# Kernel tuning notes

Measured on AMD Instinct MI355X. Metric: run time of the kernel, lower is better.

## Reference

```python
import jax, jax.numpy as jnp
import numpy as np

N, E = 10000, 160000          # nodes, support edges
CIN, COUT = 32, 32            # channels
R, B = 6, 1                   # radial rings, band limit
M = 2 * B + 1                 # angular frequencies (-B..B)
EPS = 1e-8
PI = float(np.pi)


def _cplx(a):
    # (..., 2) real -> complex64
    return jax.lax.complex(a[..., 0], a[..., 1])


def _reim(z):
    # complex -> (..., 2) real
    return jnp.stack([jnp.real(z), jnp.imag(z)], axis=-1)


def _field_conv(xc, edges, stenc, w, off):
    """FieldConv (ftype=1): real radial/angular weights with per-channel phase offsets.
    xc: (N,Cin) complex, stenc: (E,R,M) complex stencil (transport+quadrature pre-multiplied),
    w: (R,M,Cin,Cout) real, off: (Cin,Cout) phase offsets."""
    Wc = w * jax.lax.complex(jnp.cos(off), jnp.sin(off))[None, None]   # (R,M,Cin,Cout) complex
    src, tgt = edges[:, 0], edges[:, 1]
    # edge gather + complex stencil multiply: (E,R,M,Cin)
    contrib = stenc[:, :, :, None] * xc[src][:, None, None, :]
    # scatter-add to target nodes: (N,R,M,Cin)
    agg = jax.ops.segment_sum(contrib, tgt, num_segments=N)
    # dense per-node filter contraction
    return jnp.einsum('nrmc,rmcd->nd', agg, Wc)


def _tangent_nonlin(xc, b):
    # magnitude ReLU with learned bias, direction preserved (complex tangent features)
    mag = jnp.abs(xc)
    return (jax.nn.relu(mag + b) / jnp.maximum(mag, EPS)) * xc


def _forward(x, supp_edges, supp_sten, w1, off1, b1, w2, off2, b2, res_w):
    xc = _cplx(x)                # (N,CIN) complex64
    stenc = _cplx(supp_sten)     # (E,R,M) complex64
    h = _tangent_nonlin(_field_conv(xc, supp_edges, stenc, w1, off1), b1)
    h = _field_conv(h, supp_edges, stenc, w2, off2)
    y = _tangent_nonlin(xc @ _cplx(res_w) + h, b2)   # residual TangentLin + nonlin
    return _reim(y)              # (N,COUT,2) float32


def setup_inputs() -> dict:
    key = jax.random.key(0)
    ks = jax.random.split(key, 10)
    s1 = 1.0 / np.sqrt(R * M * CIN)
    s2 = 1.0 / np.sqrt(R * M * COUT)
    return {
        'x': jax.random.normal(ks[0], (N, CIN, 2), jnp.float32),
        'supp_edges': jax.random.randint(ks[1], (E, 2), 0, N),
        'supp_sten': 0.1 * jax.random.normal(ks[2], (E, R, M, 2), jnp.float32),
        'w1': s1 * jax.random.normal(ks[3], (R, M, CIN, COUT), jnp.float32),
        'off1': jax.random.uniform(ks[4], (CIN, COUT), jnp.float32, -PI, PI),
        'b1': 0.1 * jax.random.normal(ks[5], (COUT,), jnp.float32),
        'w2': s2 * jax.random.normal(ks[6], (R, M, COUT, COUT), jnp.float32),
        'off2': jax.random.uniform(ks[7], (COUT, COUT), jnp.float32, -PI, PI),
        'b2': 0.1 * jax.random.normal(ks[8], (COUT,), jnp.float32),
        'res_w': (1.0 / np.sqrt(CIN)) * jax.random.normal(ks[9], (CIN, COUT, 2), jnp.float32),
    }


def reference(x, supp_edges, supp_sten, w1, off1, b1, w2, off2, b2, res_w):
    return _forward(x, supp_edges, supp_sten, w1, off1, b1, w2, off2, b2, res_w)
```

## Files before the change

### kernel.cpp

```cpp
#include <hip/hip_runtime.h>
#include <hip/hip_bf16.h>

#define NN   10000
#define EE   160000
#define CINC 32
#define COUTC 32
#define RRR  6
#define MMM  3
#define RM   (RRR*MMM)
#define KK   (RM*CINC)
#define KE   608
#define NPB  4
#define CAP  64
#define AROW 624
#define WSZ  19456
#define EPSV 1e-8f

typedef __attribute__((ext_vector_type(8))) short bf16x8;
typedef __attribute__((ext_vector_type(4))) float f32x4;
typedef __attribute__((ext_vector_type(16))) float f32x16;

__device__ inline short f2bf(float f) {
    __hip_bfloat16 b = __float2bfloat16(f);
    union { __hip_bfloat16 b; short s; } u; u.b = b;
    return u.s;
}
__device__ inline float bf2f(unsigned short h) {
    return __uint_as_float(((unsigned)h) << 16);
}
__device__ inline uint2 packsplit(float re, float im) {
    unsigned short rh = (unsigned short)f2bf(re);
    unsigned short rl = (unsigned short)f2bf(re - bf2f(rh));
    unsigned short ih = (unsigned short)f2bf(im);
    unsigned short il = (unsigned short)f2bf(im - bf2f(ih));
    return make_uint2((unsigned)rh | ((unsigned)rl << 16),
                      (unsigned)ih | ((unsigned)il << 16));
}

__global__ void __launch_bounds__(256)
k_build(const int* __restrict__ edges, int* __restrict__ cursor,
        const float* __restrict__ w1, const float* __restrict__ off1,
        const float* __restrict__ w2, const float* __restrict__ off2,
        short* __restrict__ Wcb1, short* __restrict__ Wcb2,
        int2* __restrict__ sei,
        const float2* __restrict__ xc, uint2* __restrict__ xbf,
        const float2* __restrict__ resw)
{
    int i = blockIdx.x*blockDim.x + threadIdx.x;
    if (i < KK*COUTC) {
        int d = i & 31;
        int k = i >> 5;
        int c = k & 31;
        int r_ = k >> 5;
        int q  = (k >> 3) & 3;
        int kk = k & 7;
        int l  = q*16 + (d & 15);
        int n2 = d >> 4;
        int addr = ((r_*2 + n2)*64 + l)*8 + kk;
        float o1 = off1[c*COUTC + d];
        float o2 = off2[c*COUTC + d];
        float s1 = sinf(o1), c1 = cosf(o1);
        float s2 = sinf(o2), c2 = cosf(o2);
        Wcb1[addr]       = f2bf(w1[i]*c1);
        Wcb1[WSZ + addr] = f2bf(w1[i]*s1);
        Wcb2[addr]       = f2bf(w2[i]*c2);
        Wcb2[WSZ + addr] = f2bf(w2[i]*s2);
    }
    if (i < 1024) {
        int n2 = i >> 9;
        int l2 = (i >> 3) & 63;
        int kk = i & 7;
        int c  = ((l2 >> 4) << 3) + kk;
        int d  = (n2 << 4) + (l2 & 15);
        int addr = ((18*2 + n2)*64 + l2)*8 + kk;
        float2 rv = resw[c*COUTC + d];
        Wcb2[addr]       = f2bf(rv.x);
        Wcb2[WSZ + addr] = f2bf(rv.y);
        Wcb1[addr]       = 0;
        Wcb1[WSZ + addr] = 0;
    }
    if (i < EE) {
        int src = edges[2*i];
        int tgt = edges[2*i+1];
        int pos = atomicAdd(&cursor[tgt], 1);
        if (pos < CAP) sei[tgt*CAP + pos] = make_int2(src, i);
    }
    if (i < NN*CINC) {
        float2 v = xc[i];
        xbf[i] = packsplit(v.x, v.y);
    }
}

__global__ void __launch_bounds__(1024)
k_order(const int* __restrict__ cnts, int2* __restrict__ order2) {
    __shared__ int bins[CAP+1];
    __shared__ int suf[128];
    __shared__ int base[CAP+1];
    int t = threadIdx.x;
    if (t <= CAP) bins[t] = 0;
    __syncthreads();
    for (int n = t; n < NN; n += 1024) {
        int d = cnts[n]; if (d > CAP) d = CAP;
        atomicAdd(&bins[d], 1);
    }
    __syncthreads();
    if (t < 128) suf[t] = (t <= CAP) ? bins[t] : 0;
    __syncthreads();
    #pragma unroll
    for (int s = 1; s < 128; s <<= 1) {
        int v = 0;
        if (t < 128 && t + s < 128) v = suf[t+s];
        __syncthreads();
        if (t < 128) suf[t] += v;
        __syncthreads();
    }
    if (t <= CAP) base[t] = (t+1 < 128) ? suf[t+1] : 0;
    __syncthreads();
    for (int n = t; n < NN; n += 1024) {
        int d = cnts[n]; if (d > CAP) d = CAP;
        int r = atomicAdd(&base[d], 1);
        order2[r] = make_int2(n, d);
    }
}

template<bool FINAL>
__global__ void __launch_bounds__(256)
k_conv(const uint2* __restrict__ xbf,
       const int2* __restrict__ order2,
       const int2* __restrict__ sei,
       const float4* __restrict__ stenc4,
       const short* __restrict__ Wcb,
       const float* __restrict__ bias,
       const float2* __restrict__ xres,
       float2* __restrict__ out,
       uint2* __restrict__ outbf)
{
    __shared__ __align__(16) short aggS[2*NPB*AROW];
    __shared__ int nid[NPB];
    int t = threadIdx.x;
    int g = t >> 6;
    int l = t & 63;
    int c = l & 31;
    int oct = l >> 5;

    f32x16 Pre = (f32x16)(0.f), Pim = (f32x16)(0.f);
    int n;
    {
        int2 hdr = order2[blockIdx.x*NPB + g];
        n = hdr.x;
        int cnt = hdr.y;
        if (l == 0) nid[g] = n;
        int srcAll = 0, eidAll = 0;
        if (l < cnt) { int2 v = sei[n*CAP + l]; srcAll = v.x; eidAll = v.y; }

        bool rmok = (c < RM);
        int rmo = ((c >> 1) << 4) + ((c & 1) << 3);
        const char* sb = (const char*)stenc4;
        int ntiles = (cnt + 15) >> 4;

        union P { unsigned u[4]; short s[8]; bf16x8 v; };

        for (int ck = 0; ck < ntiles; ++ck) {
            int ebase = ck*16 + oct*8;
            float2 sv[8];
            uint2  xv[8];
            #pragma unroll
            for (int j = 0; j < 8; ++j) {
                int e = ebase + j;
                int eid = __shfl(eidAll, e, 64);
                int s   = __shfl(srcAll, e, 64);
                bool ok = rmok && (e < cnt);
                float2 vv = make_float2(0.f, 0.f);
                if (ok) vv = *(const float2*)(sb + (size_t)eid*144 + rmo);
                sv[j] = vv;
                xv[j] = xbf[(s << 5) | c];
            }
            P Are, Aim, AimN;
            #pragma unroll
            for (int j = 0; j < 8; ++j) {
                Are.s[j] = f2bf(sv[j].x);
                Aim.s[j] = f2bf(sv[j].y);
            }
            #pragma unroll
            for (int k2 = 0; k2 < 4; ++k2) AimN.u[k2] = Aim.u[k2] ^ 0x80008000u;

            P B;
            #pragma unroll
            for (int k2 = 0; k2 < 4; ++k2)
                B.u[k2] = (xv[2*k2].x & 0xffffu) | (xv[2*k2+1].x << 16);
            Pre = __builtin_amdgcn_mfma_f32_32x32x16_bf16(Are.v, B.v, Pre, 0, 0, 0);
            Pim = __builtin_amdgcn_mfma_f32_32x32x16_bf16(Aim.v, B.v, Pim, 0, 0, 0);
            #pragma unroll
            for (int k2 = 0; k2 < 4; ++k2)
                B.u[k2] = (xv[2*k2].x >> 16) | (xv[2*k2+1].x & 0xffff0000u);
            Pre = __builtin_amdgcn_mfma_f32_32x32x16_bf16(Are.v, B.v, Pre, 0, 0, 0);
            Pim = __builtin_amdgcn_mfma_f32_32x32x16_bf16(Aim.v, B.v, Pim, 0, 0, 0);
            #pragma unroll
            for (int k2 = 0; k2 < 4; ++k2)
                B.u[k2] = (xv[2*k2].y & 0xffffu) | (xv[2*k2+1].y << 16);
            Pre = __builtin_amdgcn_mfma_f32_32x32x16_bf16(AimN.v, B.v, Pre, 0, 0, 0);
            Pim = __builtin_amdgcn_mfma_f32_32x32x16_bf16(Are.v, B.v, Pim, 0, 0, 0);
            #pragma unroll
            for (int k2 = 0; k2 < 4; ++k2)
                B.u[k2] = (xv[2*k2].y >> 16) | (xv[2*k2+1].y & 0xffff0000u);
            Pre = __builtin_amdgcn_mfma_f32_32x32x16_bf16(AimN.v, B.v, Pre, 0, 0, 0);
            Pim = __builtin_amdgcn_mfma_f32_32x32x16_bf16(Are.v, B.v, Pim, 0, 0, 0);
        }

        short* aR = aggS + g*AROW;
        short* aI = aggS + NPB*AROW + g*AROW;
        #pragma unroll
        for (int reg = 0; reg < 16; ++reg) {
            int rm = (reg & 3) + 8*(reg >> 2) + 4*oct;
            if (rm < RM) {
                aR[rm*32 + c] = f2bf(Pre[reg]);
                aI[rm*32 + c] = f2bf(Pim[reg]);
            }
        }
        if (l < 32) {
            float2 xv = make_float2(0.f, 0.f);
            if (FINAL) xv = xres[(size_t)n*CINC + l];
            aR[KK + l] = f2bf(xv.x);
            aI[KK + l] = f2bf(xv.y);
        }
    }
    __syncthreads();

    int quad = l >> 4;
    int nn16 = l & 15;
    int mrow = (nn16 < NPB) ? nn16 : NPB-1;
    int rm0 = (g < 3) ? 5*g : 15;
    int nrm = (g < 3) ? 5 : 4;
    const short* aggR = aggS;
    const short* aggI = aggS + NPB*AROW;
    const short* Wr = Wcb;
    const short* Wi = Wcb + WSZ;
    int lbase = l*8;

    f32x4 Prr[2], Pii[2], Pri[2], Pir[2];
    #pragma unroll
    for (int nt = 0; nt < 2; ++nt) {
        Prr[nt] = (f32x4)(0.f); Pii[nt] = (f32x4)(0.f);
        Pri[nt] = (f32x4)(0.f); Pir[nt] = (f32x4)(0.f);
    }
    for (int r = rm0; r < rm0 + nrm; ++r) {
        int koff = r*32 + quad*8;
        bf16x8 ar = *(const bf16x8*)(aggR + mrow*AROW + koff);
        bf16x8 ai = *(const bf16x8*)(aggI + mrow*AROW + koff);
        #pragma unroll
        for (int nt = 0; nt < 2; ++nt) {
            int woff = ((r*2 + nt) << 9) + lbase;
            bf16x8 br = *(const bf16x8*)(Wr + woff);
            bf16x8 bi = *(const bf16x8*)(Wi + woff);
            Prr[nt] = __builtin_amdgcn_mfma_f32_16x16x32_bf16(ar, br, Prr[nt], 0, 0, 0);
            Pii[nt] = __builtin_amdgcn_mfma_f32_16x16x32_bf16(ai, bi, Pii[nt], 0, 0, 0);
            Pri[nt] = __builtin_amdgcn_mfma_f32_16x16x32_bf16(ar, bi, Pri[nt], 0, 0, 0);
            Pir[nt] = __builtin_amdgcn_mfma_f32_16x16x32_bf16(ai, br, Pir[nt], 0, 0, 0);
        }
    }
    __syncthreads();

    float2* dump = (float2*)aggS;
    if (quad == 0) {
        #pragma unroll
        for (int reg = 0; reg < 4; ++reg) {
            int m = reg;
            #pragma unroll
            for (int nt = 0; nt < 2; ++nt) {
                int d = nt*16 + nn16;
                dump[((size_t)g*NPB + m)*COUTC + d] =
                    make_float2(Prr[nt][reg] - Pii[nt][reg],
                                Pri[nt][reg] + Pir[nt][reg]);
            }
        }
    }
    __syncthreads();

    if (t < NPB*COUTC) {
        int m = t >> 5, d = t & 31;
        int nn = nid[m];
        float2 hv = make_float2(0.f, 0.f);
        #pragma unroll
        for (int w = 0; w < NPB; ++w) {
            float2 v = dump[((size_t)w*NPB + m)*COUTC + d];
            hv.x += v.x; hv.y += v.y;
        }
        float mag = sqrtf(hv.x*hv.x + hv.y*hv.y);
        float num = mag + bias[d]; if (num < 0.f) num = 0.f;
        float den = (mag > EPSV) ? mag : EPSV;
        float f = num / den;
        if (FINAL) out[(size_t)nn*COUTC + d] = make_float2(f*hv.x, f*hv.y);
        else       outbf[(size_t)nn*COUTC + d] = packsplit(f*hv.x, f*hv.y);
    }
}

extern "C" void kernel_launch(void* const* d_in, const int* in_sizes, int n_in,
                              void* d_out, int out_size, void* d_ws, size_t ws_size,
                              hipStream_t stream) {
    const float2* xc   = (const float2*)d_in[0];
    const int*   edges = (const int*)  d_in[1];
    const float4* stenc4 = (const float4*)d_in[2];
    const float* w1    = (const float*)d_in[3];
    const float* off1  = (const float*)d_in[4];
    const float* b1    = (const float*)d_in[5];
    const float* w2    = (const float*)d_in[6];
    const float* off2  = (const float*)d_in[7];
    const float* b2    = (const float*)d_in[8];
    const float2* resw = (const float2*)d_in[9];
    float2* out = (float2*)d_out;

    char* ws = (char*)d_ws;
    size_t o = 0;
    auto alloc = [&](size_t bytes) {
        o = (o + 255) & ~(size_t)255;
        size_t r = o; o += bytes; return r;
    };
    int*    cursor = (int*)  (ws + alloc(NN*sizeof(int)));
    int2*   order2 = (int2*) (ws + alloc(NN*sizeof(int2)));
    int2*   sei    = (int2*) (ws + alloc((size_t)NN*CAP*sizeof(int2)));
    short*  Wcb1   = (short*)(ws + alloc((size_t)2*WSZ*sizeof(short)));
    short*  Wcb2   = (short*)(ws + alloc((size_t)2*WSZ*sizeof(short)));
    uint2*  xbf    = (uint2*)(ws + alloc((size_t)NN*CINC*sizeof(uint2)));
    uint2*  hbf    = (uint2*)(ws + alloc((size_t)NN*CINC*sizeof(uint2)));
    (void)ws_size; (void)in_sizes; (void)n_in; (void)out_size;

    hipMemsetAsync(cursor, 0, NN*sizeof(int), stream);
    k_build<<<(NN*CINC + 255)/256, 256, 0, stream>>>(edges, cursor, w1, off1, w2, off2,
                                                     Wcb1, Wcb2, sei, xc, xbf, resw);
    k_order<<<1, 1024, 0, stream>>>(cursor, order2);

    k_conv<false><<<NN/NPB, 256, 0, stream>>>(xbf, order2, sei, stenc4,
                                              Wcb1, b1, nullptr, nullptr, hbf);
    k_conv<true> <<<NN/NPB, 256, 0, stream>>>(hbf, order2, sei, stenc4,
                                              Wcb2, b2, xc, out, nullptr);
}
```

Before: 149.3 us.

## Drop degree-sort kernel, prefetch edge tiles, fold complex MFMA accumulators

```diff
diff --git a/kernel.cpp b/kernel.cpp
--- a/kernel.cpp
+++ b/kernel.cpp
@@ -91,42 +91,10 @@
     }
 }
 
-__global__ void __launch_bounds__(1024)
-k_order(const int* __restrict__ cnts, int2* __restrict__ order2) {
-    __shared__ int bins[CAP+1];
-    __shared__ int suf[128];
-    __shared__ int base[CAP+1];
-    int t = threadIdx.x;
-    if (t <= CAP) bins[t] = 0;
-    __syncthreads();
-    for (int n = t; n < NN; n += 1024) {
-        int d = cnts[n]; if (d > CAP) d = CAP;
-        atomicAdd(&bins[d], 1);
-    }
-    __syncthreads();
-    if (t < 128) suf[t] = (t <= CAP) ? bins[t] : 0;
-    __syncthreads();
-    #pragma unroll
-    for (int s = 1; s < 128; s <<= 1) {
-        int v = 0;
-        if (t < 128 && t + s < 128) v = suf[t+s];
-        __syncthreads();
-        if (t < 128) suf[t] += v;
-        __syncthreads();
-    }
-    if (t <= CAP) base[t] = (t+1 < 128) ? suf[t+1] : 0;
-    __syncthreads();
-    for (int n = t; n < NN; n += 1024) {
-        int d = cnts[n]; if (d > CAP) d = CAP;
-        int r = atomicAdd(&base[d], 1);
-        order2[r] = make_int2(n, d);
-    }
-}
-
 template<bool FINAL>
-__global__ void __launch_bounds__(256)
+__global__ void __launch_bounds__(256, 4)
 k_conv(const uint2* __restrict__ xbf,
-       const int2* __restrict__ order2,
+       const int*  __restrict__ cnts,
        const int2* __restrict__ sei,
        const float4* __restrict__ stenc4,
        const short* __restrict__ Wcb,
@@ -136,22 +104,21 @@
        uint2* __restrict__ outbf)
 {
     __shared__ __align__(16) short aggS[2*NPB*AROW];
-    __shared__ int nid[NPB];
     int t = threadIdx.x;
     int g = t >> 6;
     int l = t & 63;
     int c = l & 31;
     int oct = l >> 5;
+    int n = blockIdx.x*NPB + g;
 
     f32x16 Pre = (f32x16)(0.f), Pim = (f32x16)(0.f);
-    int n;
     {
-        int2 hdr = order2[blockIdx.x*NPB + g];
-        n = hdr.x;
-        int cnt = hdr.y;
-        if (l == 0) nid[g] = n;
-        int srcAll = 0, eidAll = 0;
-        if (l < cnt) { int2 v = sei[n*CAP + l]; srcAll = v.x; eidAll = v.y; }
+        int2 v0 = make_int2(0, 0);
+        if (l < 32) v0 = sei[n*CAP + l];
+        int cnt = cnts[n]; if (cnt > CAP) cnt = CAP;
+        if (l >= 32 && l < cnt) v0 = sei[n*CAP + l];
+        int srcAll = (l < cnt) ? v0.x : 0;
+        int eidAll = (l < cnt) ? v0.y : 0;
 
         bool rmok = (c < RM);
         int rmo = ((c >> 1) << 4) + ((c & 1) << 3);
@@ -159,11 +126,11 @@
         int ntiles = (cnt + 15) >> 4;
 
         union P { unsigned u[4]; short s[8]; bf16x8 v; };
-
-        for (int ck = 0; ck < ntiles; ++ck) {
+        float2 sv[8], svn[8];
+        uint2  xv[8], xvn[8];
+
+        auto tload = [&](int ck, float2* svp, uint2* xvp) {
             int ebase = ck*16 + oct*8;
-            float2 sv[8];
-            uint2  xv[8];
             #pragma unroll
             for (int j = 0; j < 8; ++j) {
                 int e = ebase + j;
@@ -172,39 +139,53 @@
                 bool ok = rmok && (e < cnt);
                 float2 vv = make_float2(0.f, 0.f);
                 if (ok) vv = *(const float2*)(sb + (size_t)eid*144 + rmo);
-                sv[j] = vv;
-                xv[j] = xbf[(s << 5) | c];
-            }
+                svp[j] = vv;
+                xvp[j] = xbf[(s << 5) | c];
+            }
+        };
+        auto tcompute = [&](const float2* svp, const uint2* xvp) {
             P Are, Aim, AimN;
             #pragma unroll
             for (int j = 0; j < 8; ++j) {
-                Are.s[j] = f2bf(sv[j].x);
-                Aim.s[j] = f2bf(sv[j].y);
+                Are.s[j] = f2bf(svp[j].x);
+                Aim.s[j] = f2bf(svp[j].y);
             }
             #pragma unroll
             for (int k2 = 0; k2 < 4; ++k2) AimN.u[k2] = Aim.u[k2] ^ 0x80008000u;
-
             P B;
             #pragma unroll
             for (int k2 = 0; k2 < 4; ++k2)
-                B.u[k2] = (xv[2*k2].x & 0xffffu) | (xv[2*k2+1].x << 16);
+                B.u[k2] = (xvp[2*k2].x & 0xffffu) | (xvp[2*k2+1].x << 16);
             Pre = __builtin_amdgcn_mfma_f32_32x32x16_bf16(Are.v, B.v, Pre, 0, 0, 0);
             Pim = __builtin_amdgcn_mfma_f32_32x32x16_bf16(Aim.v, B.v, Pim, 0, 0, 0);
             #pragma unroll
             for (int k2 = 0; k2 < 4; ++k2)
-                B.u[k2] = (xv[2*k2].x >> 16) | (xv[2*k2+1].x & 0xffff0000u);
+                B.u[k2] = (xvp[2*k2].x >> 16) | (xvp[2*k2+1].x & 0xffff0000u);
             Pre = __builtin_amdgcn_mfma_f32_32x32x16_bf16(Are.v, B.v, Pre, 0, 0, 0);
             Pim = __builtin_amdgcn_mfma_f32_32x32x16_bf16(Aim.v, B.v, Pim, 0, 0, 0);
             #pragma unroll
             for (int k2 = 0; k2 < 4; ++k2)
-                B.u[k2] = (xv[2*k2].y & 0xffffu) | (xv[2*k2+1].y << 16);
+                B.u[k2] = (xvp[2*k2].y & 0xffffu) | (xvp[2*k2+1].y << 16);
             Pre = __builtin_amdgcn_mfma_f32_32x32x16_bf16(AimN.v, B.v, Pre, 0, 0, 0);
             Pim = __builtin_amdgcn_mfma_f32_32x32x16_bf16(Are.v, B.v, Pim, 0, 0, 0);
             #pragma unroll
             for (int k2 = 0; k2 < 4; ++k2)
-                B.u[k2] = (xv[2*k2].y >> 16) | (xv[2*k2+1].y & 0xffff0000u);
+                B.u[k2] = (xvp[2*k2].y >> 16) | (xvp[2*k2+1].y & 0xffff0000u);
             Pre = __builtin_amdgcn_mfma_f32_32x32x16_bf16(AimN.v, B.v, Pre, 0, 0, 0);
             Pim = __builtin_amdgcn_mfma_f32_32x32x16_bf16(Are.v, B.v, Pim, 0, 0, 0);
+        };
+
+        if (ntiles > 0) {
+            tload(0, sv, xv);
+            for (int ck = 0; ck < ntiles; ++ck) {
+                bool more = (ck + 1 < ntiles);
+                if (more) tload(ck+1, svn, xvn);
+                tcompute(sv, xv);
+                if (more) {
+                    #pragma unroll
+                    for (int j = 0; j < 8; ++j) { sv[j] = svn[j]; xv[j] = xvn[j]; }
+                }
+            }
         }
 
         short* aR = aggS + g*AROW;
@@ -218,10 +199,10 @@
             }
         }
         if (l < 32) {
-            float2 xv = make_float2(0.f, 0.f);
-            if (FINAL) xv = xres[(size_t)n*CINC + l];
-            aR[KK + l] = f2bf(xv.x);
-            aI[KK + l] = f2bf(xv.y);
+            float2 xvv = make_float2(0.f, 0.f);
+            if (FINAL) xvv = xres[(size_t)n*CINC + l];
+            aR[KK + l] = f2bf(xvv.x);
+            aI[KK + l] = f2bf(xvv.y);
         }
     }
     __syncthreads();
@@ -237,25 +218,26 @@
     const short* Wi = Wcb + WSZ;
     int lbase = l*8;
 
-    f32x4 Prr[2], Pii[2], Pri[2], Pir[2];
+    f32x4 Dre[2], Dim[2];
     #pragma unroll
-    for (int nt = 0; nt < 2; ++nt) {
-        Prr[nt] = (f32x4)(0.f); Pii[nt] = (f32x4)(0.f);
-        Pri[nt] = (f32x4)(0.f); Pir[nt] = (f32x4)(0.f);
-    }
+    for (int nt = 0; nt < 2; ++nt) { Dre[nt] = (f32x4)(0.f); Dim[nt] = (f32x4)(0.f); }
+    union PU { unsigned u[4]; bf16x8 v; };
     for (int r = rm0; r < rm0 + nrm; ++r) {
         int koff = r*32 + quad*8;
         bf16x8 ar = *(const bf16x8*)(aggR + mrow*AROW + koff);
-        bf16x8 ai = *(const bf16x8*)(aggI + mrow*AROW + koff);
+        PU ai, ain;
+        ai.v = *(const bf16x8*)(aggI + mrow*AROW + koff);
+        #pragma unroll
+        for (int k2 = 0; k2 < 4; ++k2) ain.u[k2] = ai.u[k2] ^ 0x80008000u;
         #pragma unroll
         for (int nt = 0; nt < 2; ++nt) {
             int woff = ((r*2 + nt) << 9) + lbase;
             bf16x8 br = *(const bf16x8*)(Wr + woff);
             bf16x8 bi = *(const bf16x8*)(Wi + woff);
-            Prr[nt] = __builtin_amdgcn_mfma_f32_16x16x32_bf16(ar, br, Prr[nt], 0, 0, 0);
-            Pii[nt] = __builtin_amdgcn_mfma_f32_16x16x32_bf16(ai, bi, Pii[nt], 0, 0, 0);
-            Pri[nt] = __builtin_amdgcn_mfma_f32_16x16x32_bf16(ar, bi, Pri[nt], 0, 0, 0);
-            Pir[nt] = __builtin_amdgcn_mfma_f32_16x16x32_bf16(ai, br, Pir[nt], 0, 0, 0);
+            Dre[nt] = __builtin_amdgcn_mfma_f32_16x16x32_bf16(ar,    br, Dre[nt], 0, 0, 0);
+            Dre[nt] = __builtin_amdgcn_mfma_f32_16x16x32_bf16(ain.v, bi, Dre[nt], 0, 0, 0);
+            Dim[nt] = __builtin_amdgcn_mfma_f32_16x16x32_bf16(ar,    bi, Dim[nt], 0, 0, 0);
+            Dim[nt] = __builtin_amdgcn_mfma_f32_16x16x32_bf16(ai.v,  br, Dim[nt], 0, 0, 0);
         }
     }
     __syncthreads();
@@ -269,8 +251,7 @@
             for (int nt = 0; nt < 2; ++nt) {
                 int d = nt*16 + nn16;
                 dump[((size_t)g*NPB + m)*COUTC + d] =
-                    make_float2(Prr[nt][reg] - Pii[nt][reg],
-                                Pri[nt][reg] + Pir[nt][reg]);
+                    make_float2(Dre[nt][reg], Dim[nt][reg]);
             }
         }
     }
@@ -278,7 +259,7 @@
 
     if (t < NPB*COUTC) {
         int m = t >> 5, d = t & 31;
-        int nn = nid[m];
+        int nn = blockIdx.x*NPB + m;
         float2 hv = make_float2(0.f, 0.f);
         #pragma unroll
         for (int w = 0; w < NPB; ++w) {
@@ -316,7 +297,6 @@
         size_t r = o; o += bytes; return r;
     };
     int*    cursor = (int*)  (ws + alloc(NN*sizeof(int)));
-    int2*   order2 = (int2*) (ws + alloc(NN*sizeof(int2)));
     int2*   sei    = (int2*) (ws + alloc((size_t)NN*CAP*sizeof(int2)));
     short*  Wcb1   = (short*)(ws + alloc((size_t)2*WSZ*sizeof(short)));
     short*  Wcb2   = (short*)(ws + alloc((size_t)2*WSZ*sizeof(short)));
@@ -327,10 +307,9 @@
     hipMemsetAsync(cursor, 0, NN*sizeof(int), stream);
     k_build<<<(NN*CINC + 255)/256, 256, 0, stream>>>(edges, cursor, w1, off1, w2, off2,
                                                      Wcb1, Wcb2, sei, xc, xbf, resw);
-    k_order<<<1, 1024, 0, stream>>>(cursor, order2);
-
-    k_conv<false><<<NN/NPB, 256, 0, stream>>>(xbf, order2, sei, stenc4,
+
+    k_conv<false><<<NN/NPB, 256, 0, stream>>>(xbf, cursor, sei, stenc4,
                                               Wcb1, b1, nullptr, nullptr, hbf);
-    k_conv<true> <<<NN/NPB, 256, 0, stream>>>(hbf, order2, sei, stenc4,
+    k_conv<true> <<<NN/NPB, 256, 0, stream>>>(hbf, cursor, sei, stenc4,
                                               Wcb2, b2, xc, out, nullptr);
 }
```

After: 139.4 us. -6.6%, faster.
